# Performance work log

Hardware: AMD Instinct MI355X
Metric: run time of the kernel (lower is better)

Reference implementation:

```python
import jax, jax.numpy as jnp
import numpy as np
from functools import partial

D_MODEL, D_INNER, D_STATE, DT_RANK, D_CONV, N_LAYER = 1024, 2048, 16, 64, 4, 4
OUT_DIM = 1024
EPS = 1e-5


def rmsnorm(x, w):
    return x * jax.lax.rsqrt(jnp.mean(x * x, axis=-1, keepdims=True) + EPS) * w


def causal_depthwise_conv(x, w, b):
    # x: [B, L, D]; w: [D, K]; depthwise causal conv along L
    xc = jnp.transpose(x, (0, 2, 1))  # [B, D, L]
    out = jax.lax.conv_general_dilated(
        xc, w[:, None, :],  # [D, 1, K]
        window_strides=(1,), padding=[(D_CONV - 1, 0)],
        dimension_numbers=('NCH', 'OIH', 'NCH'),
        feature_group_count=D_INNER)
    out = out + b[None, :, None]
    return jnp.transpose(out, (0, 2, 1))  # [B, L, D]


def selective_scan(u, delta, A, B, C, D):
    # u, delta: [b,l,d]; A: [d,n]; B,C: [b,l,n]; D: [d]
    def step(h, inp):
        d_t, B_t, C_t, u_t = inp  # [b,d],[b,n],[b,n],[b,d]
        dA = jnp.exp(d_t[..., None] * A)            # [b,d,n]
        h = dA * h + (d_t * u_t)[..., None] * B_t[:, None, :]
        y = jnp.einsum('bdn,bn->bd', h, C_t)
        return h, y
    b = u.shape[0]
    h0 = jnp.zeros((b, D_INNER, D_STATE), dtype=u.dtype)
    xs = (jnp.swapaxes(delta, 0, 1), jnp.swapaxes(B, 0, 1),
          jnp.swapaxes(C, 0, 1), jnp.swapaxes(u, 0, 1))
    _, ys = jax.lax.scan(step, h0, xs)
    y = jnp.swapaxes(ys, 0, 1)  # [b,l,d]
    return y + u * D


def mamba_block(x, in_w, conv_w, conv_b, xproj_w, dt_w, dt_b, A_log, D, out_w):
    xz = jnp.einsum('bld,ed->ble', x, in_w)            # [b,l,2*di]
    xp, z = jnp.split(xz, 2, axis=-1)
    xp = jax.nn.silu(causal_depthwise_conv(xp, conv_w, conv_b))
    x_dbl = jnp.einsum('bld,ed->ble', xp, xproj_w)      # [b,l,dt_rank+2n]
    dt, Bm, Cm = jnp.split(x_dbl, [DT_RANK, DT_RANK + D_STATE], axis=-1)
    delta = jax.nn.softplus(jnp.einsum('blr,dr->bld', dt, dt_w) + dt_b)
    A = -jnp.exp(A_log)
    y = selective_scan(xp, delta, A, Bm, Cm, D)
    y = y * jax.nn.silu(z)
    return jnp.einsum('bld,md->blm', y, out_w)


def setup_inputs() -> dict:
    key = jax.random.key(0)
    ks = jax.random.split(key, 16)
    s = 0.02
    x = jax.random.normal(ks[0], (2, 2048, D_MODEL), dtype=jnp.float32)
    emb_w = jax.random.normal(ks[1], (D_MODEL, D_MODEL), dtype=jnp.float32) * s
    emb_b = jnp.zeros((D_MODEL,), dtype=jnp.float32)
    L = N_LAYER
    in_proj_w = jax.random.normal(ks[2], (L, 2 * D_INNER, D_MODEL), dtype=jnp.float32) * s
    conv_w = jax.random.normal(ks[3], (L, D_INNER, D_CONV), dtype=jnp.float32) * 0.1
    conv_b = jnp.zeros((L, D_INNER), dtype=jnp.float32)
    x_proj_w = jax.random.normal(ks[4], (L, DT_RANK + 2 * D_STATE, D_INNER), dtype=jnp.float32) * s
    dt_proj_w = jax.random.normal(ks[5], (L, D_INNER, DT_RANK), dtype=jnp.float32) * s
    dt_proj_b = jax.random.uniform(ks[6], (L, D_INNER), dtype=jnp.float32, minval=-4.0, maxval=-2.0)
    A_log = jnp.broadcast_to(jnp.log(jnp.arange(1, D_STATE + 1, dtype=jnp.float32)), (L, D_INNER, D_STATE)).copy()
    D = jnp.ones((L, D_INNER), dtype=jnp.float32)
    out_proj_w = jax.random.normal(ks[7], (L, D_MODEL, D_INNER), dtype=jnp.float32) * s
    norm_w = jnp.ones((D_MODEL,), dtype=jnp.float32)
    head_w = jax.random.normal(ks[8], (OUT_DIM, D_MODEL), dtype=jnp.float32) * s
    return dict(x=x, emb_w=emb_w, emb_b=emb_b, in_proj_w=in_proj_w, conv_w=conv_w,
                conv_b=conv_b, x_proj_w=x_proj_w, dt_proj_w=dt_proj_w,
                dt_proj_b=dt_proj_b, A_log=A_log, D=D, out_proj_w=out_proj_w,
                norm_w=norm_w, head_w=head_w)


def reference(x, emb_w, emb_b, in_proj_w, conv_w, conv_b, x_proj_w, dt_proj_w,
              dt_proj_b, A_log, D, out_proj_w, norm_w, head_w):
    h = jnp.einsum('bli,di->bld', x, emb_w) + emb_b
    for i in range(N_LAYER):
        y = mamba_block(h, in_proj_w[i], conv_w[i], conv_b[i], x_proj_w[i],
                        dt_proj_w[i], dt_proj_b[i], A_log[i], D[i], out_proj_w[i])
        h = h + rmsnorm(y, norm_w)
    h = rmsnorm(h, norm_w)
    return jnp.einsum('bld,od->blo', h, head_w)
```

## Files before the change

kernel.cpp:

```cpp
#include <hip/hip_runtime.h>
#include <hip/hip_bf16.h>

#define DMODEL 1024
#define DINNER 2048
#define DSTATE 16
#define DTRANK 64
#define NLAYER 4
#define SEQ    2048
#define NB     2
#define BL     (NB*SEQ)

#define NCH   128
#define CLEN  (SEQ / NCH)

#define KSPLIT 8
#define NXD    96

typedef __bf16 bf16x8 __attribute__((ext_vector_type(8)));
typedef float  f32x4  __attribute__((ext_vector_type(4)));
typedef unsigned short u16x8 __attribute__((ext_vector_type(8)));

__device__ __forceinline__ unsigned short f2bf(float f) {
  unsigned int x = __builtin_bit_cast(unsigned int, f);
  x += 0x7fffu + ((x >> 16) & 1u);
  return (unsigned short)(x >> 16);
}
__device__ __forceinline__ float bf2f(unsigned short u) {
  unsigned int x = ((unsigned int)u) << 16;
  return __builtin_bit_cast(float, x);
}
__device__ __forceinline__ float siluf(float x) {
  return x * (1.f / (1.f + __expf(-x)));
}
__device__ __forceinline__ float softplusf(float x) {
  return (x > 15.f) ? x : __logf(1.f + __expf(x));
}

__device__ __forceinline__ void gload_lds16(const void* g, void* l) {
  __builtin_amdgcn_global_load_lds(
      (const __attribute__((address_space(1))) void*)g,
      (__attribute__((address_space(3))) void*)l, 16, 0, 0);
}

__device__ __forceinline__ void pack16(const float* p, u16x8& u0, u16x8& u1) {
  float4 f0 = *(const float4*)(p);
  float4 f1 = *(const float4*)(p + 4);
  float4 f2 = *(const float4*)(p + 8);
  float4 f3 = *(const float4*)(p + 12);
  u0[0]=f2bf(f0.x); u0[1]=f2bf(f0.y); u0[2]=f2bf(f0.z); u0[3]=f2bf(f0.w);
  u0[4]=f2bf(f1.x); u0[5]=f2bf(f1.y); u0[6]=f2bf(f1.z); u0[7]=f2bf(f1.w);
  u1[0]=f2bf(f2.x); u1[1]=f2bf(f2.y); u1[2]=f2bf(f2.z); u1[3]=f2bf(f2.w);
  u1[4]=f2bf(f3.x); u1[5]=f2bf(f3.y); u1[6]=f2bf(f3.z); u1[7]=f2bf(f3.w);
}

__global__ __launch_bounds__(512, 2) void gemm256(
    const unsigned short* __restrict__ A, int lda,
    const unsigned short* __restrict__ B, int ldb,
    unsigned short* __restrict__ Cbf, int ldc, int K)
{
  __shared__ alignas(16) unsigned short lds[3 * 16384];

  const int tid  = threadIdx.x;
  const int bm   = blockIdx.x, bn = blockIdx.y;
  const int wave = tid >> 6, lane = tid & 63;
  const int wm   = wave >> 2, wn = wave & 3;
  const int fr   = lane & 15, fq = lane >> 4;

  const int srow   = lane >> 2;
  const int schunk = (lane & 3) ^ ((lane >> 3) & 3);
  const unsigned short* Abase = A + (size_t)(bm * 256) * lda;
  const unsigned short* Bbase = B + (size_t)(bn * 256) * ldb;

  const int rc = fq ^ ((fr >> 1) & 3);

  f32x4 acc[8][4] = {};

#define STAGE256(t)                                                          \
  {                                                                          \
    char* sbase = (char*)lds + ((t) % 3) * 32768;                            \
    int k0 = (t) * 32;                                                       \
    _Pragma("unroll")                                                        \
    for (int r = 0; r < 2; ++r) {                                            \
      gload_lds16(Abase + (size_t)(r * 128 + wave * 16 + srow) * lda + k0 +  \
                      schunk * 8,                                            \
                  sbase + r * 8192 + wave * 1024);                           \
      gload_lds16(Bbase + (size_t)(r * 128 + wave * 16 + srow) * ldb + k0 +  \
                      schunk * 8,                                            \
                  sbase + 16384 + r * 8192 + wave * 1024);                   \
    }                                                                        \
  }

  const int NT = K >> 5;

  STAGE256(0);
  __builtin_amdgcn_sched_barrier(0);
  STAGE256(1);
  asm volatile("s_waitcnt vmcnt(4)" ::: "memory");
  __builtin_amdgcn_s_barrier();
  __builtin_amdgcn_sched_barrier(0);

  for (int t = 0; t < NT; ++t) {
    if (t + 2 < NT) STAGE256(t + 2);

    const char* bufp = (const char*)lds + (t % 3) * 32768;

    bf16x8 bfr[4];
#pragma unroll
    for (int nj = 0; nj < 4; ++nj)
      bfr[nj] = *(const bf16x8*)(bufp + 16384 +
                                 (wn * 64 + nj * 16 + fr) * 64 + rc * 16);
    __builtin_amdgcn_s_setprio(1);
#pragma unroll
    for (int mi = 0; mi < 8; ++mi) {
      bf16x8 af = *(const bf16x8*)(bufp + (wm * 128 + mi * 16 + fr) * 64 + rc * 16);
#pragma unroll
      for (int nj = 0; nj < 4; ++nj)
        acc[mi][nj] = __builtin_amdgcn_mfma_f32_16x16x32_bf16(af, bfr[nj], acc[mi][nj], 0, 0, 0);
    }
    __builtin_amdgcn_s_setprio(0);

    __builtin_amdgcn_sched_barrier(0);
    if (t + 2 < NT) {
      asm volatile("s_waitcnt vmcnt(4)" ::: "memory");
    } else if (t + 1 < NT) {
      asm volatile("s_waitcnt vmcnt(0)" ::: "memory");
    }
    __builtin_amdgcn_s_barrier();
    __builtin_amdgcn_sched_barrier(0);
  }
#undef STAGE256

#pragma unroll
  for (int mi = 0; mi < 8; ++mi)
#pragma unroll
    for (int nj = 0; nj < 4; ++nj)
#pragma unroll
      for (int q = 0; q < 4; ++q) {
        int row = bm * 256 + wm * 128 + mi * 16 + fq * 4 + q;
        int col = bn * 256 + wn * 64 + nj * 16 + fr;
        Cbf[(size_t)row * ldc + col] = f2bf(acc[mi][nj][q]);
      }
}

template<int ACT>
__global__ __launch_bounds__(256) void gemm_bf(
    const unsigned short* __restrict__ A, int lda,
    const unsigned short* __restrict__ B, int ldb,
    float* __restrict__ C, int ldc, int K,
    const float* __restrict__ bias,
    unsigned short* __restrict__ Cbf)
{
  __shared__ alignas(16) unsigned short ldsb[3 * 8192];

  const int tid  = threadIdx.x;
  const int bm   = blockIdx.x, bn = blockIdx.y;
  const int wave = tid >> 6,  lane = tid & 63;
  const int wm   = wave >> 1, wn   = wave & 1;
  const int fr   = lane & 15, fq   = lane >> 4;

  const int srow   = lane >> 2;
  const int schunk = (lane & 3) ^ ((lane >> 3) & 3);
  const unsigned short* Abase = A + (size_t)(bm * 128) * lda;
  const unsigned short* Bbase = B + (size_t)(bn * 128) * ldb;

  const int rc = fq ^ ((fr >> 1) & 3);

  f32x4 acc[4][4] = {};

#define STAGEP(t)                                                            \
  {                                                                          \
    char* sbase = (char*)ldsb + ((t) % 3) * 16384;                           \
    int k0 = (t) * 32;                                                       \
    _Pragma("unroll")                                                        \
    for (int j = 0; j < 2; ++j) {                                            \
      gload_lds16(Abase + (size_t)(wave * 32 + j * 16 + srow) * lda + k0 +   \
                      schunk * 8,                                            \
                  sbase + wave * 2048 + j * 1024);                           \
      gload_lds16(Bbase + (size_t)(wave * 32 + j * 16 + srow) * ldb + k0 +   \
                      schunk * 8,                                            \
                  sbase + 8192 + wave * 2048 + j * 1024);                    \
    }                                                                        \
  }

  const int NT = K >> 5;

  STAGEP(0);
  __builtin_amdgcn_sched_barrier(0);
  STAGEP(1);
  asm volatile("s_waitcnt vmcnt(4)" ::: "memory");
  __builtin_amdgcn_s_barrier();
  __builtin_amdgcn_sched_barrier(0);

  for (int t = 0; t < NT; ++t) {
    if (t + 2 < NT) STAGEP(t + 2);

    const char* bufp = (const char*)ldsb + (t % 3) * 16384;

    bf16x8 af[4], bfr[4];
#pragma unroll
    for (int mi = 0; mi < 4; ++mi)
      af[mi] = *(const bf16x8*)(bufp + (wm * 64 + mi * 16 + fr) * 64 + rc * 16);
#pragma unroll
    for (int nj = 0; nj < 4; ++nj)
      bfr[nj] = *(const bf16x8*)(bufp + 8192 +
                                 (wn * 64 + nj * 16 + fr) * 64 + rc * 16);
    __builtin_amdgcn_s_setprio(1);
#pragma unroll
    for (int mi = 0; mi < 4; ++mi)
#pragma unroll
      for (int nj = 0; nj < 4; ++nj)
        acc[mi][nj] = __builtin_amdgcn_mfma_f32_16x16x32_bf16(af[mi], bfr[nj], acc[mi][nj], 0, 0, 0);
    __builtin_amdgcn_s_setprio(0);

    __builtin_amdgcn_sched_barrier(0);
    if (t + 2 < NT) {
      asm volatile("s_waitcnt vmcnt(4)" ::: "memory");
    } else if (t + 1 < NT) {
      asm volatile("s_waitcnt vmcnt(0)" ::: "memory");
    }
    __builtin_amdgcn_s_barrier();
    __builtin_amdgcn_sched_barrier(0);
  }
#undef STAGEP

#pragma unroll
  for (int mi = 0; mi < 4; ++mi)
#pragma unroll
    for (int nj = 0; nj < 4; ++nj)
#pragma unroll
      for (int q = 0; q < 4; ++q) {
        int row = bm * 128 + wm * 64 + mi * 16 + fq * 4 + q;
        int col = bn * 128 + wn * 64 + nj * 16 + fr;
        float v = acc[mi][nj][q];
        if (bias) v += bias[col];
        if (ACT == 1) v = softplusf(v);
        if (C)   C[(size_t)row * ldc + col] = v;
        if (Cbf) Cbf[(size_t)row * ldc + col] = f2bf(v);
      }
}

__global__ __launch_bounds__(256) void gemm_xdbl(
    const unsigned short* __restrict__ A, const float* __restrict__ B,
    float* __restrict__ part)
{
  __shared__ alignas(16) unsigned short As[128 * 32];
  __shared__ alignas(16) unsigned short Bs[128 * 32];

  const int tid  = threadIdx.x;
  const int bm   = blockIdx.x;
  const int z    = blockIdx.z;
  const int wave = tid >> 6,  lane = tid & 63;
  const int wm   = wave >> 1, wn   = wave & 1;
  const int fr   = lane & 15, fq   = lane >> 4;

  const int r  = tid >> 1, hh = tid & 1;
  const int sw = (r & 7) << 4;
  const int offS0 = ((r * 64 + hh * 32)     ) ^ sw;
  const int offS1 = ((r * 64 + hh * 32 + 16)) ^ sw;

  const unsigned short* aRow = A + (size_t)(bm * 128 + r) * DINNER + hh * 16;
  const float* bRow = B + (size_t)r * DINNER + hh * 16;
  const bool bValid = (r < NXD);

  f32x4 acc[4][4] = {};

  const int kbeg = z * (DINNER / KSPLIT);
  for (int k0 = kbeg; k0 < kbeg + DINNER / KSPLIT; k0 += 32) {
    {
      u16x8 u0 = *(const u16x8*)(aRow + k0);
      u16x8 u1 = *(const u16x8*)(aRow + k0 + 8);
      *(u16x8*)((char*)As + offS0) = u0;
      *(u16x8*)((char*)As + offS1) = u1;
    }
    {
      u16x8 u0 = {}, u1 = {};
      if (bValid) pack16(bRow + k0, u0, u1);
      *(u16x8*)((char*)Bs + offS0) = u0;
      *(u16x8*)((char*)Bs + offS1) = u1;
    }
    __syncthreads();

    bf16x8 af[4], bfr[4];
#pragma unroll
    for (int mi = 0; mi < 4; ++mi) {
      int ra = wm * 64 + mi * 16 + fr;
      af[mi] = *(const bf16x8*)((const char*)As + ((ra * 64 + fq * 16) ^ ((ra & 7) << 4)));
    }
#pragma unroll
    for (int nj = 0; nj < 4; ++nj) {
      int rb = wn * 64 + nj * 16 + fr;
      bfr[nj] = *(const bf16x8*)((const char*)Bs + ((rb * 64 + fq * 16) ^ ((rb & 7) << 4)));
    }
#pragma unroll
    for (int mi = 0; mi < 4; ++mi)
#pragma unroll
      for (int nj = 0; nj < 4; ++nj)
        acc[mi][nj] = __builtin_amdgcn_mfma_f32_16x16x32_bf16(af[mi], bfr[nj], acc[mi][nj], 0, 0, 0);
    __syncthreads();
  }

#pragma unroll
  for (int mi = 0; mi < 4; ++mi)
#pragma unroll
    for (int nj = 0; nj < 4; ++nj)
#pragma unroll
      for (int q = 0; q < 4; ++q) {
        int row = bm * 128 + wm * 64 + mi * 16 + fq * 4 + q;
        int col = wn * 64 + nj * 16 + fr;
        if (col < NXD)
          part[((size_t)z * BL + row) * NXD + col] = acc[mi][nj][q];
      }
}

__global__ __launch_bounds__(256) void reduce_xdbl(
    const float* __restrict__ part, float* __restrict__ xdbl,
    unsigned short* __restrict__ xdbf)
{
  int i = blockIdx.x * 256 + threadIdx.x;
  float s = 0.f;
#pragma unroll
  for (int z = 0; z < KSPLIT; ++z) s += part[(size_t)z * BL * NXD + i];
  xdbl[i] = s;
  xdbf[i] = f2bf(s);
}

__global__ __launch_bounds__(256) void cvt_bf16(
    const float* __restrict__ in, unsigned short* __restrict__ out)
{
  int i = (blockIdx.x * 256 + threadIdx.x) * 4;
  float4 v = *(const float4*)(in + i);
  ushort4 o;
  o.x = f2bf(v.x); o.y = f2bf(v.y); o.z = f2bf(v.z); o.w = f2bf(v.w);
  *(ushort4*)(out + i) = o;
}

__global__ __launch_bounds__(256) void conv_silu_kernel(
    const unsigned short* __restrict__ xz, const float* __restrict__ cw,
    const float* __restrict__ cb, unsigned short* __restrict__ xpc)
{
  int idx = blockIdx.x * 256 + threadIdx.x;
  int dq  = idx & 511;
  int row = idx >> 9;
  int l   = row & (SEQ - 1);
  int d   = dq << 2;

  float4 bv = *(const float4*)(cb + d);
  float4 w0 = *(const float4*)(cw + (size_t)(d + 0) * 4);
  float4 w1 = *(const float4*)(cw + (size_t)(d + 1) * 4);
  float4 w2 = *(const float4*)(cw + (size_t)(d + 2) * 4);
  float4 w3 = *(const float4*)(cw + (size_t)(d + 3) * 4);

  float a0 = bv.x, a1 = bv.y, a2 = bv.z, a3 = bv.w;
#pragma unroll
  for (int k = 0; k < 4; ++k) {
    int ls = l - 3 + k;
    if (ls >= 0) {
      ushort4 xv = *(const ushort4*)(xz + (size_t)(row - 3 + k) * (2 * DINNER) + d);
      float x0 = bf2f(xv.x), x1 = bf2f(xv.y), x2 = bf2f(xv.z), x3 = bf2f(xv.w);
      float c0 = (k == 0) ? w0.x : (k == 1) ? w0.y : (k == 2) ? w0.z : w0.w;
      float c1 = (k == 0) ? w1.x : (k == 1) ? w1.y : (k == 2) ? w1.z : w1.w;
      float c2 = (k == 0) ? w2.x : (k == 1) ? w2.y : (k == 2) ? w2.z : w2.w;
      float c3 = (k == 0) ? w3.x : (k == 1) ? w3.y : (k == 2) ? w3.z : w3.w;
      a0 += x0 * c0; a1 += x1 * c1; a2 += x2 * c2; a3 += x3 * c3;
    }
  }
  ushort4 o;
  o.x = f2bf(siluf(a0)); o.y = f2bf(siluf(a1));
  o.z = f2bf(siluf(a2)); o.w = f2bf(siluf(a3));
  *(ushort4*)(xpc + (size_t)row * DINNER + d) = o;
}

__global__ __launch_bounds__(64) void scan_pass1(
    const unsigned short* __restrict__ dltb, const unsigned short* __restrict__ u_,
    const float* __restrict__ xd, const float* __restrict__ Alog,
    unsigned short* __restrict__ Sws, float* __restrict__ sdlws)
{
  int t = blockIdx.x * 64 + threadIdx.x;
  int d = t & (DINNER - 1);
  int cb = t >> 11;
  int c = cb & (NCH - 1);
  int b = cb / NCH;
  size_t r0 = (size_t)b * SEQ + (size_t)c * CLEN;

  float An0 = -__expf(Alog[(size_t)d * 16]);

  float S[16];
#pragma unroll
  for (int n = 0; n < 16; ++n) S[n] = 0.f;
  float sdl = 0.f;

  float dl = bf2f(dltb[r0 * DINNER + d]);
  float uu = bf2f(u_ [r0 * DINNER + d]);
  const float4* Bp0 = (const float4*)(xd + r0 * 96 + 64);
  float4 B0 = Bp0[0], B1 = Bp0[1], B2 = Bp0[2], B3 = Bp0[3];

#define P1_STEP                                                           \
  {                                                                       \
    float du = dl * uu;                                                   \
    sdl += dl;                                                            \
    float e1 = __expf(dl * An0);                                          \
    float Bv[16] = {B0.x,B0.y,B0.z,B0.w, B1.x,B1.y,B1.z,B1.w,             \
                    B2.x,B2.y,B2.z,B2.w, B3.x,B3.y,B3.z,B3.w};            \
    float p = e1;                                                         \
    _Pragma("unroll")                                                     \
    for (int n = 0; n < 16; ++n) {                                        \
      S[n] = p * S[n] + du * Bv[n];                                       \
      p *= e1;                                                            \
    }                                                                     \
  }

  for (int l = 0; l < CLEN - 1; ++l) {
    size_t rn = r0 + l + 1;
    float dln = bf2f(dltb[rn * DINNER + d]);
    float uun = bf2f(u_ [rn * DINNER + d]);
    const float4* Bp = (const float4*)(xd + rn * 96 + 64);
    float4 Bn0 = Bp[0], Bn1 = Bp[1], Bn2 = Bp[2], Bn3 = Bp[3];
    P1_STEP;
    dl = dln; uu = uun; B0 = Bn0; B1 = Bn1; B2 = Bn2; B3 = Bn3;
  }
  P1_STEP;
#undef P1_STEP

  size_t base = (size_t)cb * 16 * DINNER + d;
#pragma unroll
  for (int n = 0; n < 16; ++n) Sws[base + (size_t)n * DINNER] = f2bf(S[n]);
  sdlws[(size_t)cb * DINNER + d] = sdl;
}

__global__ __launch_bounds__(256) void scan_pass2(
    unsigned short* SH, const float* __restrict__ sdlws,
    const float* __restrict__ Alog)
{
  int t = blockIdx.x * 256 + threadIdx.x;
  int d = t & (DINNER - 1);
  int n = (t >> 11) & 15;
  int b = t >> 15;

  float Ann = -(float)(n + 1) * __expf(Alog[(size_t)d * 16]);

  float h = 0.f;

  size_t bc0 = (size_t)b * NCH;
  float sdl = sdlws[bc0 * DINNER + d];
  float Sc  = bf2f(SH[(bc0 * 16 + n) * DINNER + d]);

  for (int c = 0; c < NCH - 1; ++c) {
    size_t bcn = bc0 + c + 1;
    float sdln = sdlws[bcn * DINNER + d];
    float Scn  = bf2f(SH[(bcn * 16 + n) * DINNER + d]);
    size_t idx = ((bc0 + c) * 16 + n) * DINNER + d;
    unsigned short hout = f2bf(h);
    h = __expf(Ann * sdl) * h + Sc;
    SH[idx] = hout;
    sdl = sdln; Sc = Scn;
  }
  {
    size_t idx = ((bc0 + NCH - 1) * 16 + n) * DINNER + d;
    SH[idx] = f2bf(h);
  }
}

__global__ __launch_bounds__(64) void scan_pass3(
    const unsigned short* __restrict__ dltb,
    const unsigned short* __restrict__ u_,
    const float* __restrict__ xd,
    const unsigned short* __restrict__ xzb,
    const float* __restrict__ Alog,
    const float* __restrict__ Dv,
    const unsigned short* __restrict__ SH,
    unsigned short* __restrict__ ybf)
{
  int t = blockIdx.x * 64 + threadIdx.x;
  int d = t & (DINNER - 1);
  int cb = t >> 11;
  int c = cb & (NCH - 1);
  int b = cb / NCH;
  size_t r0 = (size_t)b * SEQ + (size_t)c * CLEN;

  float An0 = -__expf(Alog[(size_t)d * 16]);

  float h[16];
  {
    size_t base = (size_t)cb * 16 * DINNER + d;
#pragma unroll
    for (int n = 0; n < 16; ++n) h[n] = bf2f(SH[base + (size_t)n * DINNER]);
  }
  float Dd = Dv[d];

  float dl = bf2f(dltb[r0 * DINNER + d]);
  float uu = bf2f(u_ [r0 * DINNER + d]);
  float zz = bf2f(xzb[r0 * (2 * DINNER) + DINNER + d]);
  const float4* Xp0 = (const float4*)(xd + r0 * 96 + 64);
  float4 B0 = Xp0[0], B1 = Xp0[1], B2 = Xp0[2], B3 = Xp0[3];
  float4 C0 = Xp0[4], C1 = Xp0[5], C2 = Xp0[6], C3 = Xp0[7];

#define P3_STEP(RR)                                                       \
  {                                                                       \
    float Bv[16] = {B0.x,B0.y,B0.z,B0.w, B1.x,B1.y,B1.z,B1.w,             \
                    B2.x,B2.y,B2.z,B2.w, B3.x,B3.y,B3.z,B3.w};            \
    float Cv[16] = {C0.x,C0.y,C0.z,C0.w, C1.x,C1.y,C1.z,C1.w,             \
                    C2.x,C2.y,C2.z,C2.w, C3.x,C3.y,C3.z,C3.w};            \
    float du = dl * uu;                                                   \
    float e1 = __expf(dl * An0);                                          \
    float y0 = 0.f, y1 = 0.f;                                             \
    float p = e1;                                                         \
    _Pragma("unroll")                                                     \
    for (int n = 0; n < 16; n += 2) {                                     \
      h[n]   = p * h[n]   + du * Bv[n];   y0 += h[n]   * Cv[n];           \
      p *= e1;                                                            \
      h[n+1] = p * h[n+1] + du * Bv[n+1]; y1 += h[n+1] * Cv[n+1];         \
      p *= e1;                                                            \
    }                                                                     \
    float y = y0 + y1;                                                    \
    ybf[(RR) * DINNER + d] = f2bf((y + uu * Dd) * siluf(zz));             \
  }

  for (int l = 0; l < CLEN - 1; ++l) {
    size_t rn = r0 + l + 1;
    float dln = bf2f(dltb[rn * DINNER + d]);
    float uun = bf2f(u_ [rn * DINNER + d]);
    float zzn = bf2f(xzb[rn * (2 * DINNER) + DINNER + d]);
    const float4* Xp = (const float4*)(xd + rn * 96 + 64);
    float4 Bn0 = Xp[0], Bn1 = Xp[1], Bn2 = Xp[2], Bn3 = Xp[3];
    float4 Cn0 = Xp[4], Cn1 = Xp[5], Cn2 = Xp[6], Cn3 = Xp[7];
    P3_STEP(r0 + l);
    dl = dln; uu = uun; zz = zzn;
    B0 = Bn0; B1 = Bn1; B2 = Bn2; B3 = Bn3;
    C0 = Cn0; C1 = Cn1; C2 = Cn2; C3 = Cn3;
  }
  P3_STEP(r0 + CLEN - 1);
#undef P3_STEP
}

template<int ADDRES, int WF32, int WBF>
__global__ __launch_bounds__(256) void rmsnorm_kernel(
    const float* __restrict__ x, const float* __restrict__ w,
    const float* __restrict__ res, float* __restrict__ out,
    unsigned short* __restrict__ outbf)
{
  int row = blockIdx.x, tid = threadIdx.x;
  float4 v = *(const float4*)(x + (size_t)row * DMODEL + tid * 4);
  float ss = v.x * v.x + v.y * v.y + v.z * v.z + v.w * v.w;
#pragma unroll
  for (int off = 32; off > 0; off >>= 1) ss += __shfl_xor(ss, off);
  __shared__ float sb[4];
  if ((tid & 63) == 0) sb[tid >> 6] = ss;
  __syncthreads();
  ss = (sb[0] + sb[1]) + (sb[2] + sb[3]);
  float sc = rsqrtf(ss * (1.f / DMODEL) + 1e-5f);
  float4 wv = *(const float4*)(w + tid * 4);
  float4 o;
  o.x = v.x * sc * wv.x; o.y = v.y * sc * wv.y;
  o.z = v.z * sc * wv.z; o.w = v.w * sc * wv.w;
  if (ADDRES) {
    float4 rv = *(const float4*)(res + (size_t)row * DMODEL + tid * 4);
    o.x += rv.x; o.y += rv.y; o.z += rv.z; o.w += rv.w;
  }
  if (WF32) *(float4*)(out + (size_t)row * DMODEL + tid * 4) = o;
  if (WBF) {
    ushort4 ob;
    ob.x = f2bf(o.x); ob.y = f2bf(o.y); ob.z = f2bf(o.z); ob.w = f2bf(o.w);
    *(ushort4*)(outbf + (size_t)row * DMODEL + tid * 4) = ob;
  }
}

extern "C" void kernel_launch(void* const* d_in, const int* in_sizes, int n_in,
                              void* d_out, int out_size, void* d_ws, size_t ws_size,
                              hipStream_t stream) {
  const float* x        = (const float*)d_in[0];
  const float* emb_w    = (const float*)d_in[1];
  const float* emb_b    = (const float*)d_in[2];
  const float* in_projw = (const float*)d_in[3];
  const float* conv_w   = (const float*)d_in[4];
  const float* conv_b   = (const float*)d_in[5];
  const float* x_projw  = (const float*)d_in[6];
  const float* dt_projw = (const float*)d_in[7];
  const float* dt_projb = (const float*)d_in[8];
  const float* A_log    = (const float*)d_in[9];
  const float* Dvec     = (const float*)d_in[10];
  const float* out_projw= (const float*)d_in[11];
  const float* norm_w   = (const float*)d_in[12];
  const float* head_w   = (const float*)d_in[13];

  float* ws = (float*)d_ws;
  float* h    = ws;
  unsigned short* xzb = (unsigned short*)(h + (size_t)BL * DMODEL);
  unsigned short* xpcb= xzb + (size_t)BL * 2 * DINNER;
  unsigned short* dltb= xpcb+ (size_t)BL * DINNER;
  float* xdbl = (float*)(dltb + (size_t)BL * DINNER);
  unsigned short* SHb = (unsigned short*)(xdbl + (size_t)BL * NXD);
  float* sdlw = (float*)(SHb + (size_t)NB * NCH * 16 * DINNER);
  float* part = sdlw + (size_t)NB * NCH * DINNER;
  unsigned short* hbf = (unsigned short*)(part + (size_t)KSPLIT * BL * NXD);
  unsigned short* ybf = hbf + (size_t)BL * DMODEL;
  unsigned short* wInAll  = ybf + (size_t)BL * DINNER;
  unsigned short* wOutAll = wInAll + (size_t)NLAYER * 2 * DINNER * DMODEL;
  unsigned short* wDtAll  = wOutAll + (size_t)NLAYER * DMODEL * DINNER;
  unsigned short* wEmb    = wDtAll + (size_t)NLAYER * DINNER * DTRANK;
  unsigned short* wHead   = wEmb + (size_t)DMODEL * DMODEL;
  unsigned short* xdbf= SHb + (size_t)NB * NCH * 16 * DINNER - (size_t)BL * NXD;
  unsigned short* xbf = (unsigned short*)part;
  float* tmp  = (float*)xzb;

  dim3 blk(256);

  cvt_bf16<<<dim3(BL * DMODEL / 1024), blk, 0, stream>>>(x, xbf);
  cvt_bf16<<<dim3(DMODEL * DMODEL / 1024), blk, 0, stream>>>(emb_w, wEmb);
  cvt_bf16<<<dim3(NLAYER * 2 * DINNER * DMODEL / 1024), blk, 0, stream>>>(in_projw, wInAll);
  cvt_bf16<<<dim3(NLAYER * DMODEL * DINNER / 1024), blk, 0, stream>>>(out_projw, wOutAll);
  cvt_bf16<<<dim3(NLAYER * DINNER * DTRANK / 1024), blk, 0, stream>>>(dt_projw, wDtAll);
  cvt_bf16<<<dim3(DMODEL * DMODEL / 1024), blk, 0, stream>>>(head_w, wHead);

  gemm_bf<0><<<dim3(BL / 128, DMODEL / 128), blk, 0, stream>>>(
      xbf, DMODEL, wEmb, DMODEL, h, DMODEL, DMODEL, emb_b, hbf);

  for (int i = 0; i < NLAYER; ++i) {
    const unsigned short* wA = wInAll  + (size_t)i * 2 * DINNER * DMODEL;
    const unsigned short* wB = wOutAll + (size_t)i * DMODEL * DINNER;
    const unsigned short* wd = wDtAll  + (size_t)i * DINNER * DTRANK;
    const float* cw   = conv_w   + (size_t)i * DINNER * 4;
    const float* cb   = conv_b   + (size_t)i * DINNER;
    const float* xpw  = x_projw  + (size_t)i * NXD * DINNER;
    const float* dtb  = dt_projb + (size_t)i * DINNER;
    const float* Al   = A_log    + (size_t)i * DINNER * DSTATE;
    const float* Dl   = Dvec     + (size_t)i * DINNER;

    gemm256<<<dim3(BL / 256, (2 * DINNER) / 256), dim3(512), 0, stream>>>(
        hbf, DMODEL, wA, DMODEL, xzb, 2 * DINNER, DMODEL);
    conv_silu_kernel<<<dim3(BL * (DINNER / 4) / 256), blk, 0, stream>>>(xzb, cw, cb, xpcb);
    gemm_xdbl<<<dim3(BL / 128, 1, KSPLIT), blk, 0, stream>>>(xpcb, xpw, part);
    reduce_xdbl<<<dim3(BL * NXD / 256), blk, 0, stream>>>(part, xdbl, xdbf);
    gemm_bf<1><<<dim3(BL / 128, DINNER / 128), blk, 0, stream>>>(
        xdbf, NXD, wd, DTRANK, nullptr, DINNER, DTRANK, dtb, dltb);
    scan_pass1<<<dim3(NB * NCH * DINNER / 64), dim3(64), 0, stream>>>(
        dltb, xpcb, xdbl, Al, SHb, sdlw);
    scan_pass2<<<dim3(NB * 16 * DINNER / 256), blk, 0, stream>>>(SHb, sdlw, Al);
    scan_pass3<<<dim3(NB * NCH * DINNER / 64), dim3(64), 0, stream>>>(
        dltb, xpcb, xdbl, xzb, Al, Dl, SHb, ybf);
    gemm_bf<0><<<dim3(BL / 128, DMODEL / 128), blk, 0, stream>>>(
        ybf, DINNER, wB, DINNER, tmp, DMODEL, DINNER, nullptr, nullptr);
    rmsnorm_kernel<1, 1, 1><<<dim3(BL), blk, 0, stream>>>(tmp, norm_w, h, h, hbf);
  }

  rmsnorm_kernel<0, 0, 1><<<dim3(BL), blk, 0, stream>>>(h, norm_w, nullptr, nullptr, hbf);
  gemm_bf<0><<<dim3(BL / 128, DMODEL / 128), blk, 0, stream>>>(
      hbf, DMODEL, wHead, DMODEL, (float*)d_out, DMODEL, DMODEL, nullptr, nullptr);
}
```

Baseline: 1.029 ms.

## Replace split-K x_proj GEMM and reduce with padded bf16 gemm_bf; bf16 out_proj output

The x_proj weights are converted once to bf16 and padded from 96 to 128 rows. This lets the generic gemm_bf kernel compute x_dbl in a single launch, replacing the split-K kernel with per-iteration fp32-to-bf16 packing plus a separate reduction kernel. The out_proj GEMM now writes bf16 instead of fp32, and rmsnorm reads bf16, which halves that intermediate traffic. In exchange, x_proj runs with only 32 blocks over the full K of 2048, so parallelism is much lower. The out_proj result also loses precision before the norm.

New measurement: 1.063 ms. 1.03x slower.

```diff
diff --git a/kernel.cpp b/kernel.cpp
--- a/kernel.cpp
+++ b/kernel.cpp
@@ -13,8 +13,7 @@
 #define NCH   128
 #define CLEN  (SEQ / NCH)
 
-#define KSPLIT 8
-#define NXD    96
+#define NXDP  128
 
 typedef __bf16 bf16x8 __attribute__((ext_vector_type(8)));
 typedef float  f32x4  __attribute__((ext_vector_type(4)));
@@ -40,17 +39,6 @@
   __builtin_amdgcn_global_load_lds(
       (const __attribute__((address_space(1))) void*)g,
       (__attribute__((address_space(3))) void*)l, 16, 0, 0);
-}
-
-__device__ __forceinline__ void pack16(const float* p, u16x8& u0, u16x8& u1) {
-  float4 f0 = *(const float4*)(p);
-  float4 f1 = *(const float4*)(p + 4);
-  float4 f2 = *(const float4*)(p + 8);
-  float4 f3 = *(const float4*)(p + 12);
-  u0[0]=f2bf(f0.x); u0[1]=f2bf(f0.y); u0[2]=f2bf(f0.z); u0[3]=f2bf(f0.w);
-  u0[4]=f2bf(f1.x); u0[5]=f2bf(f1.y); u0[6]=f2bf(f1.z); u0[7]=f2bf(f1.w);
-  u1[0]=f2bf(f2.x); u1[1]=f2bf(f2.y); u1[2]=f2bf(f2.z); u1[3]=f2bf(f2.w);
-  u1[4]=f2bf(f3.x); u1[5]=f2bf(f3.y); u1[6]=f2bf(f3.z); u1[7]=f2bf(f3.w);
 }
 
 __global__ __launch_bounds__(512, 2) void gemm256(
@@ -239,91 +227,6 @@
       }
 }
 
-__global__ __launch_bounds__(256) void gemm_xdbl(
-    const unsigned short* __restrict__ A, const float* __restrict__ B,
-    float* __restrict__ part)
-{
-  __shared__ alignas(16) unsigned short As[128 * 32];
-  __shared__ alignas(16) unsigned short Bs[128 * 32];
-
-  const int tid  = threadIdx.x;
-  const int bm   = blockIdx.x;
-  const int z    = blockIdx.z;
-  const int wave = tid >> 6,  lane = tid & 63;
-  const int wm   = wave >> 1, wn   = wave & 1;
-  const int fr   = lane & 15, fq   = lane >> 4;
-
-  const int r  = tid >> 1, hh = tid & 1;
-  const int sw = (r & 7) << 4;
-  const int offS0 = ((r * 64 + hh * 32)     ) ^ sw;
-  const int offS1 = ((r * 64 + hh * 32 + 16)) ^ sw;
-
-  const unsigned short* aRow = A + (size_t)(bm * 128 + r) * DINNER + hh * 16;
-  const float* bRow = B + (size_t)r * DINNER + hh * 16;
-  const bool bValid = (r < NXD);
-
-  f32x4 acc[4][4] = {};
-
-  const int kbeg = z * (DINNER / KSPLIT);
-  for (int k0 = kbeg; k0 < kbeg + DINNER / KSPLIT; k0 += 32) {
-    {
-      u16x8 u0 = *(const u16x8*)(aRow + k0);
-      u16x8 u1 = *(const u16x8*)(aRow + k0 + 8);
-      *(u16x8*)((char*)As + offS0) = u0;
-      *(u16x8*)((char*)As + offS1) = u1;
-    }
-    {
-      u16x8 u0 = {}, u1 = {};
-      if (bValid) pack16(bRow + k0, u0, u1);
-      *(u16x8*)((char*)Bs + offS0) = u0;
-      *(u16x8*)((char*)Bs + offS1) = u1;
-    }
-    __syncthreads();
-
-    bf16x8 af[4], bfr[4];
-#pragma unroll
-    for (int mi = 0; mi < 4; ++mi) {
-      int ra = wm * 64 + mi * 16 + fr;
-      af[mi] = *(const bf16x8*)((const char*)As + ((ra * 64 + fq * 16) ^ ((ra & 7) << 4)));
-    }
-#pragma unroll
-    for (int nj = 0; nj < 4; ++nj) {
-      int rb = wn * 64 + nj * 16 + fr;
-      bfr[nj] = *(const bf16x8*)((const char*)Bs + ((rb * 64 + fq * 16) ^ ((rb & 7) << 4)));
-    }
-#pragma unroll
-    for (int mi = 0; mi < 4; ++mi)
-#pragma unroll
-      for (int nj = 0; nj < 4; ++nj)
-        acc[mi][nj] = __builtin_amdgcn_mfma_f32_16x16x32_bf16(af[mi], bfr[nj], acc[mi][nj], 0, 0, 0);
-    __syncthreads();
-  }
-
-#pragma unroll
-  for (int mi = 0; mi < 4; ++mi)
-#pragma unroll
-    for (int nj = 0; nj < 4; ++nj)
-#pragma unroll
-      for (int q = 0; q < 4; ++q) {
-        int row = bm * 128 + wm * 64 + mi * 16 + fq * 4 + q;
-        int col = wn * 64 + nj * 16 + fr;
-        if (col < NXD)
-          part[((size_t)z * BL + row) * NXD + col] = acc[mi][nj][q];
-      }
-}
-
-__global__ __launch_bounds__(256) void reduce_xdbl(
-    const float* __restrict__ part, float* __restrict__ xdbl,
-    unsigned short* __restrict__ xdbf)
-{
-  int i = blockIdx.x * 256 + threadIdx.x;
-  float s = 0.f;
-#pragma unroll
-  for (int z = 0; z < KSPLIT; ++z) s += part[(size_t)z * BL * NXD + i];
-  xdbl[i] = s;
-  xdbf[i] = f2bf(s);
-}
-
 __global__ __launch_bounds__(256) void cvt_bf16(
     const float* __restrict__ in, unsigned short* __restrict__ out)
 {
@@ -331,6 +234,23 @@
   float4 v = *(const float4*)(in + i);
   ushort4 o;
   o.x = f2bf(v.x); o.y = f2bf(v.y); o.z = f2bf(v.z); o.w = f2bf(v.w);
+  *(ushort4*)(out + i) = o;
+}
+
+__global__ __launch_bounds__(256) void cvt_pad_xproj(
+    const float* __restrict__ in, unsigned short* __restrict__ out)
+{
+  int i = (blockIdx.x * 256 + threadIdx.x) * 4;
+  int k = i & (DINNER - 1);
+  int r = (i / DINNER) & 127;
+  int l = i / (DINNER * 128);
+  ushort4 o;
+  if (r < 96) {
+    const float4 v = *(const float4*)(in + ((size_t)l * 96 + r) * DINNER + k);
+    o.x = f2bf(v.x); o.y = f2bf(v.y); o.z = f2bf(v.z); o.w = f2bf(v.w);
+  } else {
+    o.x = o.y = o.z = o.w = 0;
+  }
   *(ushort4*)(out + i) = o;
 }
 
@@ -391,7 +311,7 @@
 
   float dl = bf2f(dltb[r0 * DINNER + d]);
   float uu = bf2f(u_ [r0 * DINNER + d]);
-  const float4* Bp0 = (const float4*)(xd + r0 * 96 + 64);
+  const float4* Bp0 = (const float4*)(xd + r0 * NXDP + 64);
   float4 B0 = Bp0[0], B1 = Bp0[1], B2 = Bp0[2], B3 = Bp0[3];
 
 #define P1_STEP                                                           \
@@ -413,7 +333,7 @@
     size_t rn = r0 + l + 1;
     float dln = bf2f(dltb[rn * DINNER + d]);
     float uun = bf2f(u_ [rn * DINNER + d]);
-    const float4* Bp = (const float4*)(xd + rn * 96 + 64);
+    const float4* Bp = (const float4*)(xd + rn * NXDP + 64);
     float4 Bn0 = Bp[0], Bn1 = Bp[1], Bn2 = Bp[2], Bn3 = Bp[3];
     P1_STEP;
     dl = dln; uu = uun; B0 = Bn0; B1 = Bn1; B2 = Bn2; B3 = Bn3;
@@ -490,7 +410,7 @@
   float dl = bf2f(dltb[r0 * DINNER + d]);
   float uu = bf2f(u_ [r0 * DINNER + d]);
   float zz = bf2f(xzb[r0 * (2 * DINNER) + DINNER + d]);
-  const float4* Xp0 = (const float4*)(xd + r0 * 96 + 64);
+  const float4* Xp0 = (const float4*)(xd + r0 * NXDP + 64);
   float4 B0 = Xp0[0], B1 = Xp0[1], B2 = Xp0[2], B3 = Xp0[3];
   float4 C0 = Xp0[4], C1 = Xp0[5], C2 = Xp0[6], C3 = Xp0[7];
 
@@ -520,7 +440,7 @@
     float dln = bf2f(dltb[rn * DINNER + d]);
     float uun = bf2f(u_ [rn * DINNER + d]);
     float zzn = bf2f(xzb[rn * (2 * DINNER) + DINNER + d]);
-    const float4* Xp = (const float4*)(xd + rn * 96 + 64);
+    const float4* Xp = (const float4*)(xd + rn * NXDP + 64);
     float4 Bn0 = Xp[0], Bn1 = Xp[1], Bn2 = Xp[2], Bn3 = Xp[3];
     float4 Cn0 = Xp[4], Cn1 = Xp[5], Cn2 = Xp[6], Cn3 = Xp[7];
     P3_STEP(r0 + l);
@@ -532,14 +452,21 @@
 #undef P3_STEP
 }
 
-template<int ADDRES, int WF32, int WBF>
+template<int XBF, int ADDRES, int WF32, int WBF>
 __global__ __launch_bounds__(256) void rmsnorm_kernel(
-    const float* __restrict__ x, const float* __restrict__ w,
+    const float* __restrict__ xf, const unsigned short* __restrict__ xb,
+    const float* __restrict__ w,
     const float* __restrict__ res, float* __restrict__ out,
     unsigned short* __restrict__ outbf)
 {
   int row = blockIdx.x, tid = threadIdx.x;
-  float4 v = *(const float4*)(x + (size_t)row * DMODEL + tid * 4);
+  float4 v;
+  if (XBF) {
+    ushort4 u = *(const ushort4*)(xb + (size_t)row * DMODEL + tid * 4);
+    v.x = bf2f(u.x); v.y = bf2f(u.y); v.z = bf2f(u.z); v.w = bf2f(u.w);
+  } else {
+    v = *(const float4*)(xf + (size_t)row * DMODEL + tid * 4);
+  }
   float ss = v.x * v.x + v.y * v.y + v.z * v.z + v.w * v.w;
 #pragma unroll
   for (int off = 32; off > 0; off >>= 1) ss += __shfl_xor(ss, off);
@@ -588,19 +515,19 @@
   unsigned short* xpcb= xzb + (size_t)BL * 2 * DINNER;
   unsigned short* dltb= xpcb+ (size_t)BL * DINNER;
   float* xdbl = (float*)(dltb + (size_t)BL * DINNER);
-  unsigned short* SHb = (unsigned short*)(xdbl + (size_t)BL * NXD);
+  unsigned short* SHb = (unsigned short*)(xdbl + (size_t)BL * NXDP);
   float* sdlw = (float*)(SHb + (size_t)NB * NCH * 16 * DINNER);
-  float* part = sdlw + (size_t)NB * NCH * DINNER;
-  unsigned short* hbf = (unsigned short*)(part + (size_t)KSPLIT * BL * NXD);
+  unsigned short* xbf = (unsigned short*)(sdlw + (size_t)NB * NCH * DINNER);
+  unsigned short* hbf = xbf + (size_t)BL * DMODEL;
   unsigned short* ybf = hbf + (size_t)BL * DMODEL;
   unsigned short* wInAll  = ybf + (size_t)BL * DINNER;
   unsigned short* wOutAll = wInAll + (size_t)NLAYER * 2 * DINNER * DMODEL;
   unsigned short* wDtAll  = wOutAll + (size_t)NLAYER * DMODEL * DINNER;
   unsigned short* wEmb    = wDtAll + (size_t)NLAYER * DINNER * DTRANK;
   unsigned short* wHead   = wEmb + (size_t)DMODEL * DMODEL;
-  unsigned short* xdbf= SHb + (size_t)NB * NCH * 16 * DINNER - (size_t)BL * NXD;
-  unsigned short* xbf = (unsigned short*)part;
-  float* tmp  = (float*)xzb;
+  unsigned short* wXpAll  = wHead + (size_t)DMODEL * DMODEL;
+  unsigned short* xdbf= SHb + (size_t)NB * NCH * 16 * DINNER - (size_t)BL * NXDP;
+  unsigned short* tmpb= xzb;
 
   dim3 blk(256);
 
@@ -610,6 +537,7 @@
   cvt_bf16<<<dim3(NLAYER * DMODEL * DINNER / 1024), blk, 0, stream>>>(out_projw, wOutAll);
   cvt_bf16<<<dim3(NLAYER * DINNER * DTRANK / 1024), blk, 0, stream>>>(dt_projw, wDtAll);
   cvt_bf16<<<dim3(DMODEL * DMODEL / 1024), blk, 0, stream>>>(head_w, wHead);
+  cvt_pad_xproj<<<dim3(NLAYER * 128 * DINNER / 1024), blk, 0, stream>>>(x_projw, wXpAll);
 
   gemm_bf<0><<<dim3(BL / 128, DMODEL / 128), blk, 0, stream>>>(
       xbf, DMODEL, wEmb, DMODEL, h, DMODEL, DMODEL, emb_b, hbf);
@@ -618,9 +546,9 @@
     const unsigned short* wA = wInAll  + (size_t)i * 2 * DINNER * DMODEL;
     const unsigned short* wB = wOutAll + (size_t)i * DMODEL * DINNER;
     const unsigned short* wd = wDtAll  + (size_t)i * DINNER * DTRANK;
+    const unsigned short* wx = wXpAll  + (size_t)i * 128 * DINNER;
     const float* cw   = conv_w   + (size_t)i * DINNER * 4;
     const float* cb   = conv_b   + (size_t)i * DINNER;
-    const float* xpw  = x_projw  + (size_t)i * NXD * DINNER;
     const float* dtb  = dt_projb + (size_t)i * DINNER;
     const float* Al   = A_log    + (size_t)i * DINNER * DSTATE;
     const float* Dl   = Dvec     + (size_t)i * DINNER;
@@ -628,21 +556,23 @@
     gemm256<<<dim3(BL / 256, (2 * DINNER) / 256), dim3(512), 0, stream>>>(
         hbf, DMODEL, wA, DMODEL, xzb, 2 * DINNER, DMODEL);
     conv_silu_kernel<<<dim3(BL * (DINNER / 4) / 256), blk, 0, stream>>>(xzb, cw, cb, xpcb);
-    gemm_xdbl<<<dim3(BL / 128, 1, KSPLIT), blk, 0, stream>>>(xpcb, xpw, part);
-    reduce_xdbl<<<dim3(BL * NXD / 256), blk, 0, stream>>>(part, xdbl, xdbf);
+    gemm_bf<0><<<dim3(BL / 128, 1), blk, 0, stream>>>(
+        xpcb, DINNER, wx, DINNER, xdbl, NXDP, DINNER, nullptr, xdbf);
     gemm_bf<1><<<dim3(BL / 128, DINNER / 128), blk, 0, stream>>>(
-        xdbf, NXD, wd, DTRANK, nullptr, DINNER, DTRANK, dtb, dltb);
+        xdbf, NXDP, wd, DTRANK, nullptr, DINNER, DTRANK, dtb, dltb);
     scan_pass1<<<dim3(NB * NCH * DINNER / 64), dim3(64), 0, stream>>>(
         dltb, xpcb, xdbl, Al, SHb, sdlw);
     scan_pass2<<<dim3(NB * 16 * DINNER / 256), blk, 0, stream>>>(SHb, sdlw, Al);
     scan_pass3<<<dim3(NB * NCH * DINNER / 64), dim3(64), 0, stream>>>(
         dltb, xpcb, xdbl, xzb, Al, Dl, SHb, ybf);
     gemm_bf<0><<<dim3(BL / 128, DMODEL / 128), blk, 0, stream>>>(
-        ybf, DINNER, wB, DINNER, tmp, DMODEL, DINNER, nullptr, nullptr);
-    rmsnorm_kernel<1, 1, 1><<<dim3(BL), blk, 0, stream>>>(tmp, norm_w, h, h, hbf);
-  }
-
-  rmsnorm_kernel<0, 0, 1><<<dim3(BL), blk, 0, stream>>>(h, norm_w, nullptr, nullptr, hbf);
+        ybf, DINNER, wB, DINNER, nullptr, DMODEL, DINNER, nullptr, tmpb);
+    rmsnorm_kernel<1, 1, 1, 1><<<dim3(BL), blk, 0, stream>>>(
+        nullptr, tmpb, norm_w, h, h, hbf);
+  }
+
+  rmsnorm_kernel<0, 0, 0, 1><<<dim3(BL), blk, 0, stream>>>(
+      h, nullptr, norm_w, nullptr, nullptr, hbf);
   gemm_bf<0><<<dim3(BL / 128, DMODEL / 128), blk, 0, stream>>>(
       hbf, DMODEL, wHead, DMODEL, (float*)d_out, DMODEL, DMODEL, nullptr, nullptr);
 }
```
